# Kernel tuning notes

Measured on AMD Instinct MI355X. Metric: run time of the kernel, lower is better.

Reference implementation:

```python
import jax, jax.numpy as jnp
import numpy as np

B, S, D = 8, 4096, 1536
NUM_ORGANISMS = 4
OUT = 2048


def setup_inputs() -> dict:
    key = jax.random.key(0)
    k_x, k_idx, k_w = jax.random.split(key, 3)
    x = jax.random.normal(k_x, (B, S, D), dtype=jnp.float32)
    organism_index = jax.random.randint(k_idx, (B,), 0, NUM_ORGANISMS, dtype=jnp.int32)
    # TruncatedNormal(stddev=1/sqrt(D)) init; plain normal*stddev is a faithful stand-in
    stddev = 1.0 / np.sqrt(D)
    w = jax.random.normal(k_w, (NUM_ORGANISMS, D, OUT), dtype=jnp.float32) * stddev
    b = jnp.zeros((NUM_ORGANISMS, OUT), dtype=jnp.float32)
    return {"x": x, "organism_index": organism_index, "w": w, "b": b}


def reference(x, organism_index, w, b):
    # Gather per-batch organism weights/biases (hard routing), then batched matmul.
    w_b = w[organism_index]          # [B, D, OUT]
    b_b = b[organism_index]          # [B, OUT]
    out = jnp.einsum('bsi,bij->bsj', x, w_b,
                     preferred_element_type=jnp.float32)  # [B, S, OUT]
    return out + b_b[:, None, :]
```

## Files before the change

kernel.cpp:

```cpp
#include <hip/hip_runtime.h>
#include <hip/hip_bf16.h>
#include <stdint.h>

#define B_    8
#define S_    4096
#define D_    1536
#define ORG_  4
#define OUT_  2048

typedef __bf16 bf16;
typedef __attribute__((ext_vector_type(8)))  bf16  bf16x8;
typedef __attribute__((ext_vector_type(4)))  float f32x4n;
typedef __attribute__((ext_vector_type(16))) float f32x16;

#define BK64 64
#define NKT  (D_ / BK64)

#define XBLKS 2048
#define WTBLK (ORG_ * (OUT_/32) * (D_/32))

__global__ void k_cvt_all(const float* __restrict__ x, bf16* __restrict__ xb,
                          const float* __restrict__ w, bf16* __restrict__ wt) {
  __shared__ float tile[32][33];
  const int bx = blockIdx.x;
  const int tid = threadIdx.x;

  if (bx < XBLKS) {
    const long n8 = (long)B_ * S_ * D_ / 8;
    long i = (long)bx * blockDim.x + tid;
    const long stride = (long)XBLKS * blockDim.x;
    for (; i < n8; i += stride) {
      const f32x4n* p = (const f32x4n*)(x + i * 8);
      f32x4n a = __builtin_nontemporal_load(p);
      f32x4n b = __builtin_nontemporal_load(p + 1);
      bf16x8 v;
      v[0] = (bf16)a[0]; v[1] = (bf16)a[1]; v[2] = (bf16)a[2]; v[3] = (bf16)a[3];
      v[4] = (bf16)b[0]; v[5] = (bf16)b[1]; v[6] = (bf16)b[2]; v[7] = (bf16)b[3];
      *(bf16x8*)(xb + i * 8) = v;
    }
  } else {
    const int q   = bx - XBLKS;
    const int org = q / ((OUT_/32) * (D_/32));
    const int rem = q % ((OUT_/32) * (D_/32));
    const int d0  = (rem / (OUT_/32)) * 32;
    const int n0  = (rem % (OUT_/32)) * 32;
    const int tx = tid & 31, ty = tid >> 5;
    const float* wsrc = w + (size_t)org * D_ * OUT_;
    bf16* wdst = wt + (size_t)org * OUT_ * D_;
#pragma unroll
    for (int j = 0; j < 32; j += 8)
      tile[ty + j][tx] = __builtin_nontemporal_load(
          wsrc + (size_t)(d0 + ty + j) * OUT_ + (n0 + tx));
    __syncthreads();
#pragma unroll
    for (int j = 0; j < 32; j += 8)
      wdst[(size_t)(n0 + ty + j) * D_ + (d0 + tx)] = (bf16)tile[tx][ty + j];
  }
}

__global__ __launch_bounds__(512, 2)
void k_gemm256(const bf16* __restrict__ xb, const bf16* __restrict__ wt,
               const int* __restrict__ oidx, const float* __restrict__ bias,
               float* __restrict__ out) {
  __shared__ __align__(16) char smem[131072];
  char* const ldsA = smem;
  char* const ldsB = smem + 65536;

  const int batch = blockIdx.y;
  const int bx = blockIdx.x;
  const int swz = (bx & 7) * 16 + (bx >> 3);
  const int tn = swz >> 4, tm = swz & 15;
  const int m0 = tm * 256, n0 = tn * 256;
  const int org = oidx[batch];

  const bf16* Ag = xb + (size_t)batch * S_ * D_ + (size_t)m0 * D_;
  const bf16* Bg = wt + (size_t)org * OUT_ * D_ + (size_t)n0 * D_;

  const int tid  = threadIdx.x;
  const int lane = tid & 63, wv = tid >> 6;
  const int wr = wv >> 2, wc = wv & 3;
  const int l31 = lane & 31, hi = lane >> 5;

  const int xorv = ((lane & 7) ^ ((lane >> 3) & 3)) << 4;
  const int off[4] = { (0  + hi * 16) ^ xorv, (32 + hi * 16) ^ xorv,
                       (64 + hi * 16) ^ xorv, (96 + hi * 16) ^ xorv };
  const int arow = (wr * 128 + l31) * 128;
  const int brow = (wc * 64  + l31) * 128;

  const int srow = tid >> 3;
  const int scol = (((tid & 7) ^ ((tid >> 3) & 7) ^ ((tid >> 6) & 3))) << 3;
  const int soff = wv * 1024;

#define LDA(v, mt, ks) (*(const bf16x8*)(ldsA + (v)*32768 + arow + (mt)*4096 + off[ks]))
#define LDB(v, nt, ks) (*(const bf16x8*)(ldsB + (v)*32768 + brow + (nt)*4096 + off[ks]))

#define STAGE_HALF(gptr, ldsbase, h, kb) do {                                            \
    __builtin_amdgcn_global_load_lds(                                                    \
      (__attribute__((address_space(1))) void*)((gptr) + (size_t)((h)*128 + srow) * D_ + (kb) + scol), \
      (__attribute__((address_space(3))) void*)((ldsbase) + (h)*16384 + soff), 16, 0, 0);\
    __builtin_amdgcn_global_load_lds(                                                    \
      (__attribute__((address_space(1))) void*)((gptr) + (size_t)((h)*128 + 64 + srow) * D_ + (kb) + scol), \
      (__attribute__((address_space(3))) void*)((ldsbase) + (h)*16384 + 8192 + soff), 16, 0, 0); \
  } while (0)

#define SBAR()  __builtin_amdgcn_s_barrier()
#define LGK0()  asm volatile("s_waitcnt lgkmcnt(0)" ::: "memory")
#define VMC4()  asm volatile("s_waitcnt vmcnt(4)" ::: "memory")
#define VMC0()  asm volatile("s_waitcnt vmcnt(0)" ::: "memory")
#define PRIO(p) __builtin_amdgcn_s_setprio(p)

  bf16x8 a[2][4], b0[4], b1[4];
  f32x16 acc[4][2];
#pragma unroll
  for (int mt = 0; mt < 4; ++mt)
#pragma unroll
    for (int nt = 0; nt < 2; ++nt)
#pragma unroll
      for (int rr = 0; rr < 16; ++rr) acc[mt][nt][rr] = 0.f;

#define READ_A2(v, mbase) do { _Pragma("unroll") for (int mm = 0; mm < 2; ++mm) \
    _Pragma("unroll") for (int ks = 0; ks < 4; ++ks) \
      a[mm][ks] = LDA(v, (mbase) + mm, ks); } while (0)
#define READ_B4(v, nt, bb) do { _Pragma("unroll") for (int ks = 0; ks < 4; ++ks) \
      bb[ks] = LDB(v, nt, ks); } while (0)
#define MFMA_O(mbase, nt, bb) do { \
    _Pragma("unroll") for (int mm = 0; mm < 2; ++mm) \
    _Pragma("unroll") for (int ks = 0; ks < 4; ++ks) \
      acc[(mbase)+mm][nt] = __builtin_amdgcn_mfma_f32_32x32x16_bf16( \
          a[mm][ks], bb[ks], acc[(mbase)+mm][nt], 0, 0, 0); } while (0)

  STAGE_HALF(Bg, ldsB, 0, 0);
  STAGE_HALF(Bg, ldsB, 1, 0);
  STAGE_HALF(Ag, ldsA, 0, 0);
  STAGE_HALF(Ag, ldsA, 1, 0);
  STAGE_HALF(Bg, ldsB + 32768, 0, BK64);
  STAGE_HALF(Bg, ldsB + 32768, 1, BK64);
  VMC4();
  SBAR();

  for (int i = 0; i < NKT / 2; ++i) {
    const int k1 = (2 * i + 1) * BK64;
    int t2 = 2 * i + 2; if (t2 > NKT - 1) t2 = NKT - 1;
    int t3 = 2 * i + 3; if (t3 > NKT - 1) t3 = NKT - 1;
    const int k2 = t2 * BK64, k3 = t3 * BK64;

    READ_A2(0, 0); READ_B4(0, 0, b0);
    STAGE_HALF(Ag, ldsA + 32768, 0, k1);
    PRIO(1); MFMA_O(0, 0, b0); PRIO(0);
    LGK0(); SBAR();
    READ_B4(0, 1, b1);
    STAGE_HALF(Ag, ldsA + 32768, 1, k1);
    PRIO(1); MFMA_O(0, 1, b1); PRIO(0);
    LGK0(); SBAR();
    READ_A2(0, 2);
    STAGE_HALF(Bg, ldsB, 0, k2);
    PRIO(1); MFMA_O(2, 0, b0); PRIO(0);
    LGK0(); SBAR();
    STAGE_HALF(Bg, ldsB, 1, k2);
    PRIO(1); MFMA_O(2, 1, b1); PRIO(0);
    VMC4();
    SBAR();
    READ_A2(1, 0); READ_B4(1, 0, b0);
    STAGE_HALF(Ag, ldsA, 0, k2);
    PRIO(1); MFMA_O(0, 0, b0); PRIO(0);
    LGK0(); SBAR();
    READ_B4(1, 1, b1);
    STAGE_HALF(Ag, ldsA, 1, k2);
    PRIO(1); MFMA_O(0, 1, b1); PRIO(0);
    LGK0(); SBAR();
    READ_A2(1, 2);
    STAGE_HALF(Bg, ldsB + 32768, 0, k3);
    PRIO(1); MFMA_O(2, 0, b0); PRIO(0);
    LGK0(); SBAR();
    STAGE_HALF(Bg, ldsB + 32768, 1, k3);
    PRIO(1); MFMA_O(2, 1, b1); PRIO(0);
    VMC4();
    SBAR();
  }

  VMC0();

  float* Og = out + (size_t)batch * S_ * OUT_ + (size_t)m0 * OUT_ + n0;
  const float* bbase = bias + (size_t)org * OUT_ + n0;
#pragma unroll
  for (int nt = 0; nt < 2; ++nt) {
    const int col = wc * 64 + nt * 32 + l31;
    const float bv = bbase[col];
#pragma unroll
    for (int mt = 0; mt < 4; ++mt) {
#pragma unroll
      for (int rr = 0; rr < 16; ++rr) {
        const int row = wr * 128 + mt * 32 + 4 * hi + (rr & 3) + 8 * (rr >> 2);
        Og[(size_t)row * OUT_ + col] = acc[mt][nt][rr] + bv;
      }
    }
  }
#undef LDA
#undef LDB
#undef STAGE_HALF
#undef SBAR
#undef LGK0
#undef VMC4
#undef VMC0
#undef PRIO
#undef READ_A2
#undef READ_B4
#undef MFMA_O
}

__global__ void k_gemm_fallback(const float* __restrict__ x, const int* __restrict__ oidx,
                                const float* __restrict__ w, const float* __restrict__ bias,
                                float* __restrict__ out) {
  const int b = blockIdx.z;
  const int org = oidx[b];
  const int n = blockIdx.x * 64 + threadIdx.x;
  const int m = blockIdx.y * 4 + threadIdx.y;
  const float* xr = x + ((size_t)b * S_ + m) * D_;
  const float* wp = w + (size_t)org * D_ * OUT_ + n;
  float acc = 0.f;
  for (int k = 0; k < D_; ++k) acc += xr[k] * wp[(size_t)k * OUT_];
  out[((size_t)b * S_ + m) * OUT_ + n] = acc + bias[(size_t)org * OUT_ + n];
}

extern "C" void kernel_launch(void* const* d_in, const int* in_sizes, int n_in,
                              void* d_out, int out_size, void* d_ws, size_t ws_size,
                              hipStream_t stream) {
  const float* x    = (const float*)d_in[0];
  const int*   oidx = (const int*)d_in[1];
  const float* w    = (const float*)d_in[2];
  const float* bias = (const float*)d_in[3];
  float* out = (float*)d_out;

  const size_t xb_elems = (size_t)B_ * S_ * D_;
  const size_t wt_elems = (size_t)ORG_ * OUT_ * D_;
  const size_t need = (xb_elems + wt_elems) * sizeof(bf16);

  if (ws_size < need) {
    dim3 g(OUT_ / 64, S_ / 4, B_);
    k_gemm_fallback<<<g, dim3(64, 4), 0, stream>>>(x, oidx, w, bias, out);
    return;
  }

  bf16* xb = (bf16*)d_ws;
  bf16* wt = xb + xb_elems;

  k_cvt_all<<<XBLKS + WTBLK, 256, 0, stream>>>(x, xb, w, wt);
  dim3 gg(128, B_);
  k_gemm256<<<gg, 512, 0, stream>>>(xb, wt, oidx, bias, out);
}
```

Before: 274.3 us.

## Coarsen GEMM pipeline phases, peel final k-iteration, and remap tile swizzle

```diff
diff --git a/kernel.cpp b/kernel.cpp
--- a/kernel.cpp
+++ b/kernel.cpp
@@ -69,7 +69,7 @@
   const int batch = blockIdx.y;
   const int bx = blockIdx.x;
   const int swz = (bx & 7) * 16 + (bx >> 3);
-  const int tn = swz >> 4, tm = swz & 15;
+  const int tm = swz >> 3, tn = swz & 7;
   const int m0 = tm * 256, n0 = tn * 256;
   const int org = oidx[batch];
 
@@ -103,6 +103,9 @@
       (__attribute__((address_space(3))) void*)((ldsbase) + (h)*16384 + 8192 + soff), 16, 0, 0); \
   } while (0)
 
+#define STAGE_TILE(gptr, ldsbase, kb) do { \
+    STAGE_HALF(gptr, ldsbase, 0, kb); STAGE_HALF(gptr, ldsbase, 1, kb); } while (0)
+
 #define SBAR()  __builtin_amdgcn_s_barrier()
 #define LGK0()  asm volatile("s_waitcnt lgkmcnt(0)" ::: "memory")
 #define VMC4()  asm volatile("s_waitcnt vmcnt(4)" ::: "memory")
@@ -124,61 +127,58 @@
 #define READ_B4(v, nt, bb) do { _Pragma("unroll") for (int ks = 0; ks < 4; ++ks) \
       bb[ks] = LDB(v, nt, ks); } while (0)
 #define MFMA_O(mbase, nt, bb) do { \
+    _Pragma("unroll") for (int ks = 0; ks < 4; ++ks) \
     _Pragma("unroll") for (int mm = 0; mm < 2; ++mm) \
-    _Pragma("unroll") for (int ks = 0; ks < 4; ++ks) \
       acc[(mbase)+mm][nt] = __builtin_amdgcn_mfma_f32_32x32x16_bf16( \
           a[mm][ks], bb[ks], acc[(mbase)+mm][nt], 0, 0, 0); } while (0)
 
-  STAGE_HALF(Bg, ldsB, 0, 0);
-  STAGE_HALF(Bg, ldsB, 1, 0);
-  STAGE_HALF(Ag, ldsA, 0, 0);
-  STAGE_HALF(Ag, ldsA, 1, 0);
-  STAGE_HALF(Bg, ldsB + 32768, 0, BK64);
-  STAGE_HALF(Bg, ldsB + 32768, 1, BK64);
+  STAGE_TILE(Bg, ldsB, 0);
+  STAGE_TILE(Ag, ldsA, 0);
+  STAGE_TILE(Bg, ldsB + 32768, BK64);
   VMC4();
   SBAR();
 
-  for (int i = 0; i < NKT / 2; ++i) {
+  for (int i = 0; i < NKT / 2 - 1; ++i) {
     const int k1 = (2 * i + 1) * BK64;
-    int t2 = 2 * i + 2; if (t2 > NKT - 1) t2 = NKT - 1;
-    int t3 = 2 * i + 3; if (t3 > NKT - 1) t3 = NKT - 1;
-    const int k2 = t2 * BK64, k3 = t3 * BK64;
-
-    READ_A2(0, 0); READ_B4(0, 0, b0);
-    STAGE_HALF(Ag, ldsA + 32768, 0, k1);
-    PRIO(1); MFMA_O(0, 0, b0); PRIO(0);
-    LGK0(); SBAR();
-    READ_B4(0, 1, b1);
-    STAGE_HALF(Ag, ldsA + 32768, 1, k1);
-    PRIO(1); MFMA_O(0, 1, b1); PRIO(0);
+    const int k2 = (2 * i + 2) * BK64;
+    const int k3 = (2 * i + 3) * BK64;
+
+    READ_A2(0, 0); READ_B4(0, 0, b0); READ_B4(0, 1, b1);
+    STAGE_TILE(Ag, ldsA + 32768, k1);
+    PRIO(1); MFMA_O(0, 0, b0); MFMA_O(0, 1, b1); PRIO(0);
     LGK0(); SBAR();
     READ_A2(0, 2);
-    STAGE_HALF(Bg, ldsB, 0, k2);
-    PRIO(1); MFMA_O(2, 0, b0); PRIO(0);
-    LGK0(); SBAR();
-    STAGE_HALF(Bg, ldsB, 1, k2);
-    PRIO(1); MFMA_O(2, 1, b1); PRIO(0);
+    STAGE_TILE(Bg, ldsB, k2);
+    PRIO(1); MFMA_O(2, 0, b0); MFMA_O(2, 1, b1); PRIO(0);
     VMC4();
     SBAR();
-    READ_A2(1, 0); READ_B4(1, 0, b0);
-    STAGE_HALF(Ag, ldsA, 0, k2);
-    PRIO(1); MFMA_O(0, 0, b0); PRIO(0);
-    LGK0(); SBAR();
-    READ_B4(1, 1, b1);
-    STAGE_HALF(Ag, ldsA, 1, k2);
-    PRIO(1); MFMA_O(0, 1, b1); PRIO(0);
+    READ_A2(1, 0); READ_B4(1, 0, b0); READ_B4(1, 1, b1);
+    STAGE_TILE(Ag, ldsA, k2);
+    PRIO(1); MFMA_O(0, 0, b0); MFMA_O(0, 1, b1); PRIO(0);
     LGK0(); SBAR();
     READ_A2(1, 2);
-    STAGE_HALF(Bg, ldsB + 32768, 0, k3);
-    PRIO(1); MFMA_O(2, 0, b0); PRIO(0);
-    LGK0(); SBAR();
-    STAGE_HALF(Bg, ldsB + 32768, 1, k3);
-    PRIO(1); MFMA_O(2, 1, b1); PRIO(0);
+    STAGE_TILE(Bg, ldsB + 32768, k3);
+    PRIO(1); MFMA_O(2, 0, b0); MFMA_O(2, 1, b1); PRIO(0);
     VMC4();
     SBAR();
   }
 
-  VMC0();
+  {
+    const int k1 = (NKT - 1) * BK64;
+    READ_A2(0, 0); READ_B4(0, 0, b0); READ_B4(0, 1, b1);
+    STAGE_TILE(Ag, ldsA + 32768, k1);
+    PRIO(1); MFMA_O(0, 0, b0); MFMA_O(0, 1, b1); PRIO(0);
+    LGK0(); SBAR();
+    READ_A2(0, 2);
+    PRIO(1); MFMA_O(2, 0, b0); MFMA_O(2, 1, b1); PRIO(0);
+    VMC0();
+    SBAR();
+    READ_A2(1, 0); READ_B4(1, 0, b0); READ_B4(1, 1, b1);
+    PRIO(1); MFMA_O(0, 0, b0); MFMA_O(0, 1, b1); PRIO(0);
+    LGK0(); SBAR();
+    READ_A2(1, 2);
+    PRIO(1); MFMA_O(2, 0, b0); MFMA_O(2, 1, b1); PRIO(0);
+  }
 
   float* Og = out + (size_t)batch * S_ * OUT_ + (size_t)m0 * OUT_ + n0;
   const float* bbase = bias + (size_t)org * OUT_ + n0;
@@ -198,6 +198,7 @@
 #undef LDA
 #undef LDB
 #undef STAGE_HALF
+#undef STAGE_TILE
 #undef SBAR
 #undef LGK0
 #undef VMC4
```

After: 265.0 us. 3.4% less time.
